# Kernel optimization log

Hardware: AMD Instinct MI355X
Metric: run time of the kernel (lower is better)

The kernel has to match this reference:

```python
import jax, jax.numpy as jnp
import numpy as np

N = 100000   # nodes
E = 1600000  # edges
Q = 500000   # query edges
F = 128      # num_features
H = 256      # hidden_dim
D = 128      # embedding_dim


def setup_inputs() -> dict:
    key = jax.random.key(0)
    ks = jax.random.split(key, 16)

    def lin_w(k, fan_in, fan_out):
        return (jax.random.normal(k, (fan_in, fan_out), jnp.float32)
                / np.float32(np.sqrt(fan_in)))

    inp = {}
    inp['x'] = jax.random.normal(ks[0], (N, F), jnp.float32)
    inp['edge_index'] = jax.random.randint(ks[1], (2, E), 0, N)
    inp['query_edges'] = jax.random.randint(ks[2], (2, Q), 0, N)
    inp['int_values'] = jax.random.randint(ks[3], (N,), 0, 1000000)
    inp['partition_ids'] = jax.random.randint(ks[4], (N,), 0, 1000)
    # GCNConv1 / GCNConv2 / encoder fc
    inp['W1'] = lin_w(ks[5], F, H);  inp['b1'] = jnp.zeros((H,), jnp.float32)
    inp['W2'] = lin_w(ks[6], H, H);  inp['b2'] = jnp.zeros((H,), jnp.float32)
    inp['Wfc'] = lin_w(ks[7], H, D); inp['bfc'] = jnp.zeros((D,), jnp.float32)
    # decoder MLP: in = 2*D + 2
    inp['Wd1'] = lin_w(ks[8], 2 * D + 2, H);    inp['bd1'] = jnp.zeros((H,), jnp.float32)
    inp['Wd2'] = lin_w(ks[9], H, H // 2);       inp['bd2'] = jnp.zeros((H // 2,), jnp.float32)
    inp['Wd3'] = lin_w(ks[10], H // 2, 1);      inp['bd3'] = jnp.zeros((1,), jnp.float32)
    return inp


def reference(x, edge_index, query_edges, int_values, partition_ids,
              W1, b1, W2, b2, Wfc, bfc, Wd1, bd1, Wd2, bd2, Wd3, bd3):
    n = x.shape[0]
    # GCN: add self-loops, symmetric degree normalization
    loop = jnp.arange(n)
    src = jnp.concatenate([edge_index[0], loop])  # [E+N]
    dst = jnp.concatenate([edge_index[1], loop])
    deg = jax.ops.segment_sum(jnp.ones_like(dst, jnp.float32), dst, num_segments=n)
    dinv = jnp.where(deg > 0, jax.lax.rsqrt(deg), 0.0)
    norm = dinv[src] * dinv[dst]  # [E+N]

    def gcn_conv(h, W, b):
        hw = h @ W                                   # [N,out]
        msg = hw[src] * norm[:, None]                # [E+N,out]
        return jax.ops.segment_sum(msg, dst, num_segments=n) + b

    h = jax.nn.relu(gcn_conv(x, W1, b1))
    h = jax.nn.relu(gcn_conv(h, W2, b2))
    z = h @ Wfc + bfc                                # [N,D]

    qs, qd = query_edges[0], query_edges[1]
    z_src = z[qs]                                    # [Q,D]
    z_dst = z[qd]
    int_diff = (int_values[qd] - int_values[qs]).astype(jnp.float32)[:, None]
    same_part = (partition_ids[qs] == partition_ids[qd]).astype(jnp.float32)[:, None]
    zc = jnp.concatenate([z_src, z_dst, int_diff, same_part], axis=-1)  # [Q,2D+2]

    u = jax.nn.relu(zc @ Wd1 + bd1)
    u = jax.nn.relu(u @ Wd2 + bd2)
    out = jax.nn.sigmoid(u @ Wd3 + bd3)
    return out.squeeze(-1)  # [Q]
```

## Files before the change

### kernel.cpp

```cpp
#include <hip/hip_runtime.h>
#include <math.h>


typedef __attribute__((ext_vector_type(8))) short short8;
typedef __attribute__((ext_vector_type(4))) float f32x4;

__device__ __forceinline__ float4 ld4(const float* p){ return *reinterpret_cast<const float4*>(p); }
__device__ __forceinline__ void st4(float* p, float4 v){ *reinterpret_cast<float4*>(p) = v; }
__device__ __forceinline__ unsigned short f2bf(float f){
    union{float f; unsigned u;} v; v.f = f;
    unsigned r = (v.u + 0x7FFFu + ((v.u >> 16) & 1u)) >> 16;
    return (unsigned short)r;
}
__device__ __forceinline__ float bf2f(unsigned short b){
    union{unsigned u; float f;} v; v.u = ((unsigned)b) << 16; return v.f;
}

__global__ void k_count(const int* __restrict__ ei, int E, int* __restrict__ counts){
    int e = blockIdx.x * 256 + threadIdx.x;
    if (e < E) atomicAdd(&counts[ei[E + e]], 1);
}

__global__ __launch_bounds__(1024) void k_blocksum(const int* __restrict__ counts, int n,
                                                   int* __restrict__ bsum){
    __shared__ int sb[1024];
    int i = blockIdx.x * 1024 + threadIdx.x;
    sb[threadIdx.x] = (i < n) ? counts[i] : 0;
    __syncthreads();
    for (int off = 512; off > 0; off >>= 1){
        if (threadIdx.x < off) sb[threadIdx.x] += sb[threadIdx.x + off];
        __syncthreads();
    }
    if (threadIdx.x == 0) bsum[blockIdx.x] = sb[0];
}

__global__ void k_bscan(const int* __restrict__ bsum, int nb,
                        int* __restrict__ boff, int* __restrict__ offsets, int n){
    if (threadIdx.x == 0){
        int run = 0;
        for (int b = 0; b < nb; ++b){ boff[b] = run; run += bsum[b]; }
        offsets[n] = run;
    }
}

__global__ __launch_bounds__(1024) void k_offsets(const int* __restrict__ counts, int n,
                                                  const int* __restrict__ boff,
                                                  int* __restrict__ offsets,
                                                  int* __restrict__ cursor,
                                                  float* __restrict__ dinv){
    __shared__ int sb[1024];
    int i = blockIdx.x * 1024 + threadIdx.x;
    int v = (i < n) ? counts[i] : 0;
    if (i < n) dinv[i] = rsqrtf((float)(v + 1));
    sb[threadIdx.x] = v;
    __syncthreads();
    for (int off = 1; off < 1024; off <<= 1){
        int t = (threadIdx.x >= off) ? sb[threadIdx.x - off] : 0;
        __syncthreads();
        sb[threadIdx.x] += t;
        __syncthreads();
    }
    if (i < n){
        int ex = boff[blockIdx.x] + sb[threadIdx.x] - v;
        offsets[i] = ex; cursor[i] = ex;
    }
}

__global__ void k_fill(const int* __restrict__ ei, int E,
                       int* __restrict__ cursor, int* __restrict__ srclist){
    int e = blockIdx.x * 256 + threadIdx.x;
    if (e < E){
        int s = ei[e], d = ei[E + e];
        int pos = atomicAdd(&cursor[d], 1);
        srclist[pos] = s;
    }
}

__global__ void k_split_w(const float* __restrict__ W, unsigned short* __restrict__ hi,
                          unsigned short* __restrict__ lo, int K, int Nn){
    int id = blockIdx.x * 256 + threadIdx.x;
    if (id >= K * Nn) return;
    int n = id / K, k = id - n * K;
    float v = W[(size_t)k * Nn + n];
    unsigned short h = f2bf(v);
    hi[id] = h;
    lo[id] = f2bf(v - bf2f(h));
}

__global__ void k_split_pack(const float* __restrict__ W, unsigned short* __restrict__ hi,
                             unsigned short* __restrict__ lo, int K, int Nn){
    int idx = blockIdx.x * 256 + threadIdx.x;
    if (idx >= K * Nn) return;
    int j = idx & 7;
    int lane = (idx >> 3) & 63;
    int frag = idx >> 9;
    int kgroups = K >> 5;
    int kg = frag % kgroups;
    int cg = frag / kgroups;
    int c = cg * 16 + (lane & 15);
    int k = kg * 32 + (lane >> 4) * 8 + j;
    float v = W[(size_t)k * Nn + c];
    unsigned short h = f2bf(v);
    hi[idx] = h;
    lo[idx] = f2bf(v - bf2f(h));
}

__global__ void k_scalerows(const float* __restrict__ x, const float* __restrict__ dinv,
                            float* __restrict__ xs, int total4){
    int id = blockIdx.x * 256 + threadIdx.x;
    if (id >= total4) return;
    int node = id >> 5;
    float d = dinv[node];
    float4 v = ld4(&x[(size_t)id * 4]);
    st4(&xs[(size_t)id * 4], make_float4(v.x*d, v.y*d, v.z*d, v.w*d));
}

__global__ __launch_bounds__(256) void k_agg2(const float* __restrict__ in,
        const int* __restrict__ offsets, const int* __restrict__ srclist,
        const float* __restrict__ dinv, float* __restrict__ out, int n){
    int wid = (blockIdx.x * 256 + threadIdx.x) >> 6;
    int lane = threadIdx.x & 63;
    if (wid >= n) return;
    int f = lane * 2;
    float2 acc = *reinterpret_cast<const float2*>(&in[(size_t)wid * 128 + f]);
    int o0 = offsets[wid], o1 = offsets[wid + 1];
    int e = o0;
    for (; e + 3 < o1; e += 4){
        int s0 = srclist[e], s1 = srclist[e+1], s2 = srclist[e+2], s3 = srclist[e+3];
        float2 v0 = *reinterpret_cast<const float2*>(&in[(size_t)s0 * 128 + f]);
        float2 v1 = *reinterpret_cast<const float2*>(&in[(size_t)s1 * 128 + f]);
        float2 v2 = *reinterpret_cast<const float2*>(&in[(size_t)s2 * 128 + f]);
        float2 v3 = *reinterpret_cast<const float2*>(&in[(size_t)s3 * 128 + f]);
        acc.x += (v0.x + v1.x) + (v2.x + v3.x);
        acc.y += (v0.y + v1.y) + (v2.y + v3.y);
    }
    for (; e < o1; ++e){
        int s0 = srclist[e];
        float2 v0 = *reinterpret_cast<const float2*>(&in[(size_t)s0 * 128 + f]);
        acc.x += v0.x; acc.y += v0.y;
    }
    float d = dinv[wid];
    *reinterpret_cast<float2*>(&out[(size_t)wid * 128 + f]) = make_float2(acc.x * d, acc.y * d);
}

__global__ __launch_bounds__(256) void k_agg4(const float* __restrict__ in,
        const int* __restrict__ offsets, const int* __restrict__ srclist,
        const float* __restrict__ dinv, float* __restrict__ out, int n){
    int wid = (blockIdx.x * 256 + threadIdx.x) >> 6;
    int lane = threadIdx.x & 63;
    if (wid >= n) return;
    int f = lane * 4;
    float4 acc = ld4(&in[(size_t)wid * 256 + f]);
    int o0 = offsets[wid], o1 = offsets[wid + 1];
    int e = o0;
    for (; e + 3 < o1; e += 4){
        int s0 = srclist[e], s1 = srclist[e+1], s2 = srclist[e+2], s3 = srclist[e+3];
        float4 v0 = ld4(&in[(size_t)s0 * 256 + f]);
        float4 v1 = ld4(&in[(size_t)s1 * 256 + f]);
        float4 v2 = ld4(&in[(size_t)s2 * 256 + f]);
        float4 v3 = ld4(&in[(size_t)s3 * 256 + f]);
        acc.x += (v0.x + v1.x) + (v2.x + v3.x);
        acc.y += (v0.y + v1.y) + (v2.y + v3.y);
        acc.z += (v0.z + v1.z) + (v2.z + v3.z);
        acc.w += (v0.w + v1.w) + (v2.w + v3.w);
    }
    for (; e < o1; ++e){
        int s0 = srclist[e];
        float4 v0 = ld4(&in[(size_t)s0 * 256 + f]);
        acc.x += v0.x; acc.y += v0.y; acc.z += v0.z; acc.w += v0.w;
    }
    float d = dinv[wid];
    st4(&out[(size_t)wid * 256 + f],
        make_float4(acc.x * d, acc.y * d, acc.z * d, acc.w * d));
}

template<bool RELU, bool POSTSCALE>
__global__ __launch_bounds__(256) void k_mgemm(
        const float* __restrict__ A, const unsigned short* __restrict__ Bh,
        const unsigned short* __restrict__ Bl, const float* __restrict__ bias,
        const float* __restrict__ pscale, float* __restrict__ C,
        int M, int K, int Nn){
    __shared__ unsigned short As_h[128][40], As_l[128][40];
    __shared__ unsigned short Bs_h[128][40], Bs_l[128][40];
    int tid = threadIdx.x;
    int l = tid & 63, w = tid >> 6;
    int wr = w >> 1, wc = w & 1;
    int row0 = blockIdx.x * 128, col0 = blockIdx.y * 128;
    int lr = l & 15, lg = l >> 4, lk = lg * 8;

    f32x4 acc[4][4] = {};

    for (int kt = 0; kt < K; kt += 32){
#pragma unroll
        for (int lp = 0; lp < 4; ++lp){
            int idx = tid + lp * 256;
            int r = idx >> 3, c4 = idx & 7;
            float4 v = make_float4(0.f, 0.f, 0.f, 0.f);
            if (row0 + r < M) v = ld4(&A[(size_t)(row0 + r) * K + kt + c4 * 4]);
            unsigned short h0 = f2bf(v.x), h1 = f2bf(v.y), h2 = f2bf(v.z), h3 = f2bf(v.w);
            unsigned short e0 = f2bf(v.x - bf2f(h0)), e1 = f2bf(v.y - bf2f(h1));
            unsigned short e2 = f2bf(v.z - bf2f(h2)), e3 = f2bf(v.w - bf2f(h3));
            *reinterpret_cast<uint2*>(&As_h[r][c4 * 4]) =
                make_uint2((unsigned)h0 | ((unsigned)h1 << 16), (unsigned)h2 | ((unsigned)h3 << 16));
            *reinterpret_cast<uint2*>(&As_l[r][c4 * 4]) =
                make_uint2((unsigned)e0 | ((unsigned)e1 << 16), (unsigned)e2 | ((unsigned)e3 << 16));
        }
#pragma unroll
        for (int lp = 0; lp < 2; ++lp){
            int idx = tid + lp * 256;
            int r = idx >> 2, c8 = idx & 3;
            size_t go = (size_t)(col0 + r) * K + kt + c8 * 8;
            *reinterpret_cast<uint4*>(&Bs_h[r][c8 * 8]) = *reinterpret_cast<const uint4*>(&Bh[go]);
            *reinterpret_cast<uint4*>(&Bs_l[r][c8 * 8]) = *reinterpret_cast<const uint4*>(&Bl[go]);
        }
        __syncthreads();

        short8 ah[4], al[4], bh[4], bl[4];
#pragma unroll
        for (int mi = 0; mi < 4; ++mi){
            ah[mi] = *reinterpret_cast<const short8*>(&As_h[wr * 64 + mi * 16 + lr][lk]);
            al[mi] = *reinterpret_cast<const short8*>(&As_l[wr * 64 + mi * 16 + lr][lk]);
        }
#pragma unroll
        for (int ni = 0; ni < 4; ++ni){
            bh[ni] = *reinterpret_cast<const short8*>(&Bs_h[wc * 64 + ni * 16 + lr][lk]);
            bl[ni] = *reinterpret_cast<const short8*>(&Bs_l[wc * 64 + ni * 16 + lr][lk]);
        }
#pragma unroll
        for (int mi = 0; mi < 4; ++mi)
#pragma unroll
            for (int ni = 0; ni < 4; ++ni)
                acc[mi][ni] = __builtin_amdgcn_mfma_f32_16x16x32_bf16(ah[mi], bh[ni], acc[mi][ni], 0, 0, 0);
#pragma unroll
        for (int mi = 0; mi < 4; ++mi)
#pragma unroll
            for (int ni = 0; ni < 4; ++ni)
                acc[mi][ni] = __builtin_amdgcn_mfma_f32_16x16x32_bf16(ah[mi], bl[ni], acc[mi][ni], 0, 0, 0);
#pragma unroll
        for (int mi = 0; mi < 4; ++mi)
#pragma unroll
            for (int ni = 0; ni < 4; ++ni)
                acc[mi][ni] = __builtin_amdgcn_mfma_f32_16x16x32_bf16(al[mi], bh[ni], acc[mi][ni], 0, 0, 0);
        __syncthreads();
    }

#pragma unroll
    for (int ni = 0; ni < 4; ++ni){
        int col = col0 + wc * 64 + ni * 16 + lr;
        float bv = bias[col];
#pragma unroll
        for (int mi = 0; mi < 4; ++mi){
#pragma unroll
            for (int rr = 0; rr < 4; ++rr){
                int grow = row0 + wr * 64 + mi * 16 + lg * 4 + rr;
                if (grow < M){
                    float v = acc[mi][ni][rr] + bv;
                    if (RELU) v = fmaxf(v, 0.f);
                    if (POSTSCALE) v *= pscale[grow];
                    C[(size_t)grow * Nn + col] = v;
                }
            }
        }
    }
}

__global__ __launch_bounds__(512, 4) void k_dec(
        const float* __restrict__ z, const int* __restrict__ qe,
        const int* __restrict__ iv, const int* __restrict__ pid,
        const unsigned short* __restrict__ W1h, const unsigned short* __restrict__ W1l,
        const float* __restrict__ Wd1, const float* __restrict__ bd1,
        const unsigned short* __restrict__ W2h, const unsigned short* __restrict__ W2l,
        const float* __restrict__ bd2, const float* __restrict__ Wd3,
        const float* __restrict__ bd3, float* __restrict__ out, int Q){
    __shared__ unsigned short As_h[64][264];
    __shared__ unsigned short As_l[64][264];
    __shared__ int   sQs[64], sQd[64];
    __shared__ float sIdf[64], sSp[64];

    int tid = threadIdx.x;
    int q0 = blockIdx.x * 64;
    if (tid < 64){
        int q = q0 + tid;
        int qs = 0, qd = 0; float idf = 0.f, sp = 0.f;
        if (q < Q){
            qs = qe[q]; qd = qe[Q + q];
            idf = (float)(iv[qd] - iv[qs]);
            sp = (pid[qs] == pid[qd]) ? 1.f : 0.f;
        }
        sQs[tid] = qs; sQd[tid] = qd; sIdf[tid] = idf; sSp[tid] = sp;
    }
    __syncthreads();

#pragma unroll
    for (int lp = 0; lp < 4; ++lp){
        int ch = tid + lp * 512;
        int r = ch >> 5, c8 = ch & 31;
        int srow = (c8 < 16) ? sQs[r] : sQd[r];
        int colb = (c8 & 15) * 8;
        float4 v0 = ld4(&z[(size_t)srow * 128 + colb]);
        float4 v1 = ld4(&z[(size_t)srow * 128 + colb + 4]);
        float vv[8] = {v0.x, v0.y, v0.z, v0.w, v1.x, v1.y, v1.z, v1.w};
        unsigned short hh[8], ll[8];
#pragma unroll
        for (int j = 0; j < 8; ++j){
            hh[j] = f2bf(vv[j]);
            ll[j] = f2bf(vv[j] - bf2f(hh[j]));
        }
        *reinterpret_cast<uint4*>(&As_h[r][c8 * 8]) = *reinterpret_cast<uint4*>(hh);
        *reinterpret_cast<uint4*>(&As_l[r][c8 * 8]) = *reinterpret_cast<uint4*>(ll);
    }
    __syncthreads();

    int l = tid & 63, w = tid >> 6;
    int wr = w >> 2, wc = w & 3;
    int lr = l & 15, lg = l >> 4, lk = lg * 8;

    f32x4 acc1[2][4] = {};
#pragma unroll
    for (int ks = 0; ks < 8; ++ks){
        int kt = ks * 32;
        short8 ah[2], al[2], bh[4], bl[4];
#pragma unroll
        for (int mi = 0; mi < 2; ++mi){
            int row = wr * 32 + mi * 16 + lr;
            ah[mi] = *reinterpret_cast<const short8*>(&As_h[row][kt + lk]);
            al[mi] = *reinterpret_cast<const short8*>(&As_l[row][kt + lk]);
        }
#pragma unroll
        for (int ni = 0; ni < 4; ++ni){
            size_t off = ((size_t)((wc * 4 + ni) * 8 + ks) << 9) + l * 8;
            bh[ni] = *reinterpret_cast<const short8*>(&W1h[off]);
            bl[ni] = *reinterpret_cast<const short8*>(&W1l[off]);
        }
#pragma unroll
        for (int mi = 0; mi < 2; ++mi)
#pragma unroll
            for (int ni = 0; ni < 4; ++ni)
                acc1[mi][ni] = __builtin_amdgcn_mfma_f32_16x16x32_bf16(ah[mi], bh[ni], acc1[mi][ni], 0, 0, 0);
#pragma unroll
        for (int mi = 0; mi < 2; ++mi)
#pragma unroll
            for (int ni = 0; ni < 4; ++ni)
                acc1[mi][ni] = __builtin_amdgcn_mfma_f32_16x16x32_bf16(ah[mi], bl[ni], acc1[mi][ni], 0, 0, 0);
#pragma unroll
        for (int mi = 0; mi < 2; ++mi)
#pragma unroll
            for (int ni = 0; ni < 4; ++ni)
                acc1[mi][ni] = __builtin_amdgcn_mfma_f32_16x16x32_bf16(al[mi], bh[ni], acc1[mi][ni], 0, 0, 0);
    }
    __syncthreads();

#pragma unroll
    for (int ni = 0; ni < 4; ++ni){
        int c = wc * 64 + ni * 16 + lr;
        float bv  = bd1[c];
        float wiv = Wd1[256 * 256 + c];
        float wsv = Wd1[257 * 256 + c];
#pragma unroll
        for (int mi = 0; mi < 2; ++mi){
#pragma unroll
            for (int rr = 0; rr < 4; ++rr){
                int r = wr * 32 + mi * 16 + lg * 4 + rr;
                float u = acc1[mi][ni][rr] + bv + sIdf[r] * wiv + sSp[r] * wsv;
                u = fmaxf(u, 0.f);
                unsigned short h = f2bf(u);
                As_h[r][c] = h;
                As_l[r][c] = f2bf(u - bf2f(h));
            }
        }
    }
    __syncthreads();

    f32x4 acc2[2][2] = {};
#pragma unroll
    for (int ks = 0; ks < 8; ++ks){
        int kt = ks * 32;
        short8 ah[2], al[2], bh[2], bl[2];
#pragma unroll
        for (int mi = 0; mi < 2; ++mi){
            int row = wr * 32 + mi * 16 + lr;
            ah[mi] = *reinterpret_cast<const short8*>(&As_h[row][kt + lk]);
            al[mi] = *reinterpret_cast<const short8*>(&As_l[row][kt + lk]);
        }
#pragma unroll
        for (int ni = 0; ni < 2; ++ni){
            size_t off = ((size_t)((wc * 2 + ni) * 8 + ks) << 9) + l * 8;
            bh[ni] = *reinterpret_cast<const short8*>(&W2h[off]);
            bl[ni] = *reinterpret_cast<const short8*>(&W2l[off]);
        }
#pragma unroll
        for (int mi = 0; mi < 2; ++mi)
#pragma unroll
            for (int ni = 0; ni < 2; ++ni)
                acc2[mi][ni] = __builtin_amdgcn_mfma_f32_16x16x32_bf16(ah[mi], bh[ni], acc2[mi][ni], 0, 0, 0);
#pragma unroll
        for (int mi = 0; mi < 2; ++mi)
#pragma unroll
            for (int ni = 0; ni < 2; ++ni)
                acc2[mi][ni] = __builtin_amdgcn_mfma_f32_16x16x32_bf16(ah[mi], bl[ni], acc2[mi][ni], 0, 0, 0);
#pragma unroll
        for (int mi = 0; mi < 2; ++mi)
#pragma unroll
            for (int ni = 0; ni < 2; ++ni)
                acc2[mi][ni] = __builtin_amdgcn_mfma_f32_16x16x32_bf16(al[mi], bh[ni], acc2[mi][ni], 0, 0, 0);
    }
    __syncthreads();

    float* red = (float*)&As_h[0][0];
    float psum[2][4] = {};
#pragma unroll
    for (int ni = 0; ni < 2; ++ni){
        int c = wc * 32 + ni * 16 + lr;
        float b2v = bd2[c];
        float w3v = Wd3[c];
#pragma unroll
        for (int mi = 0; mi < 2; ++mi)
#pragma unroll
            for (int rr = 0; rr < 4; ++rr)
                psum[mi][rr] += fmaxf(acc2[mi][ni][rr] + b2v, 0.f) * w3v;
    }
#pragma unroll
    for (int mi = 0; mi < 2; ++mi)
#pragma unroll
        for (int rr = 0; rr < 4; ++rr){
            int r = wr * 32 + mi * 16 + lg * 4 + rr;
            red[r * 65 + wc * 16 + lr] = psum[mi][rr];
        }
    __syncthreads();

    {
        int qr = tid >> 3, part = tid & 7;
        float s = 0.f;
#pragma unroll
        for (int j = 0; j < 8; ++j) s += red[qr * 65 + part * 8 + j];
        s += __shfl_xor(s, 1, 8);
        s += __shfl_xor(s, 2, 8);
        s += __shfl_xor(s, 4, 8);
        int q = q0 + qr;
        if (part == 0 && q < Q) out[q] = 1.f / (1.f + expf(-(s + bd3[0])));
    }
}

extern "C" void kernel_launch(void* const* d_in, const int* in_sizes, int n_in,
                              void* d_out, int out_size, void* d_ws, size_t ws_size,
                              hipStream_t stream){
    const float* x   = (const float*)d_in[0];
    const int*   ei  = (const int*)  d_in[1];
    const int*   qe  = (const int*)  d_in[2];
    const int*   iv  = (const int*)  d_in[3];
    const int*   pid = (const int*)  d_in[4];
    const float* W1  = (const float*)d_in[5];
    const float* b1  = (const float*)d_in[6];
    const float* W2  = (const float*)d_in[7];
    const float* b2  = (const float*)d_in[8];
    const float* Wfc = (const float*)d_in[9];
    const float* bfc = (const float*)d_in[10];
    const float* Wd1 = (const float*)d_in[11];
    const float* bd1 = (const float*)d_in[12];
    const float* Wd2 = (const float*)d_in[13];
    const float* bd2 = (const float*)d_in[14];
    const float* Wd3 = (const float*)d_in[15];
    const float* bd3 = (const float*)d_in[16];
    float* out = (float*)d_out;

    const int N = in_sizes[3];
    const int E = in_sizes[1] / 2;
    const int Q = in_sizes[2] / 2;

    char* p = (char*)d_ws;
    auto alloc = [&](size_t bytes) -> char* {
        char* r = p; p += (bytes + 255) & ~(size_t)255; return r;
    };
    int*   counts  = (int*)  alloc((size_t)N * 4);
    int*   offsets = (int*)  alloc((size_t)(N + 1) * 4);
    int*   cursor  = (int*)  alloc((size_t)(N + 1) * 4);
    int*   srclist = (int*)  alloc((size_t)E * 4);
    float* dinv    = (float*)alloc((size_t)N * 4);
    int*   bsum    = (int*)  alloc(1024 * 4);
    int*   boff    = (int*)  alloc(1024 * 4);
    unsigned short* w1h  = (unsigned short*)alloc(256 * 128 * 2);
    unsigned short* w1l  = (unsigned short*)alloc(256 * 128 * 2);
    unsigned short* w2h  = (unsigned short*)alloc(256 * 256 * 2);
    unsigned short* w2l  = (unsigned short*)alloc(256 * 256 * 2);
    unsigned short* wfh  = (unsigned short*)alloc(128 * 256 * 2);
    unsigned short* wfl  = (unsigned short*)alloc(128 * 256 * 2);
    unsigned short* wd1h = (unsigned short*)alloc(256 * 256 * 2);
    unsigned short* wd1l = (unsigned short*)alloc(256 * 256 * 2);
    unsigned short* wd2h = (unsigned short*)alloc(128 * 256 * 2);
    unsigned short* wd2l = (unsigned short*)alloc(128 * 256 * 2);
    float* P1 = (float*)alloc((size_t)N * 256 * 4);
    float* P2 = (float*)alloc((size_t)N * 256 * 4);

    float* xs  = P2;
    float* ag1 = P2 + (size_t)N * 128;
    float* h1s = P1;
    float* ag2 = P2;
    float* h2  = P1;
    float* z   = P2;

    const int nb = (N + 1023) / 1024;
    dim3 blk(256);

    hipMemsetAsync(counts, 0, (size_t)N * 4, stream);
    k_count   <<<dim3((E + 255) / 256), blk,        0, stream>>>(ei, E, counts);
    k_blocksum<<<dim3(nb),              dim3(1024), 0, stream>>>(counts, N, bsum);
    k_bscan   <<<dim3(1),               dim3(64),   0, stream>>>(bsum, nb, boff, offsets, N);
    k_offsets <<<dim3(nb),              dim3(1024), 0, stream>>>(counts, N, boff, offsets, cursor, dinv);
    k_fill    <<<dim3((E + 255) / 256), blk,        0, stream>>>(ei, E, cursor, srclist);

    k_split_w   <<<dim3(128), blk, 0, stream>>>(W1,  w1h,  w1l,  128, 256);
    k_split_w   <<<dim3(256), blk, 0, stream>>>(W2,  w2h,  w2l,  256, 256);
    k_split_w   <<<dim3(128), blk, 0, stream>>>(Wfc, wfh,  wfl,  256, 128);
    k_split_pack<<<dim3(256), blk, 0, stream>>>(Wd1, wd1h, wd1l, 256, 256);
    k_split_pack<<<dim3(128), blk, 0, stream>>>(Wd2, wd2h, wd2l, 256, 128);

    k_scalerows<<<dim3((N * 32 + 255) / 256), blk, 0, stream>>>(x, dinv, xs, N * 32);
    k_agg2<<<dim3(N / 4), blk, 0, stream>>>(xs, offsets, srclist, dinv, ag1, N);
    k_mgemm<true,  true ><<<dim3((N + 127) / 128, 2), blk, 0, stream>>>(ag1, w1h, w1l, b1, dinv, h1s, N, 128, 256);
    k_agg4<<<dim3(N / 4), blk, 0, stream>>>(h1s, offsets, srclist, dinv, ag2, N);
    k_mgemm<true,  false><<<dim3((N + 127) / 128, 2), blk, 0, stream>>>(ag2, w2h, w2l, b2, nullptr, h2, N, 256, 256);
    k_mgemm<false, false><<<dim3((N + 127) / 128, 1), blk, 0, stream>>>(h2, wfh, wfl, bfc, nullptr, z, N, 256, 128);

    k_dec<<<dim3((Q + 63) / 64), dim3(512), 0, stream>>>(z, qe, iv, pid,
                                                         wd1h, wd1l, Wd1, bd1,
                                                         wd2h, wd2l, bd2, Wd3, bd3, out, Q);
}
```

Baseline: 1.220 ms.

## Emit split-bf16 hi/lo activations from producers and fold row scaling into aggregation

Aggregation and GEMM kernels now write activations already split into bf16 hi/lo halves, so the consuming GEMMs and decoder load packed bf16 directly instead of reconverting fp32 every tile. The separate row-scaling kernel is removed and the source-degree scaling moves into the first aggregation's gather loop. This cuts redundant conversion work and one full pass over x. In exchange, the first aggregation does an extra dinv gather per edge, and the intermediate buffer layout is rearranged.

```diff
diff --git a/kernel.cpp b/kernel.cpp
--- a/kernel.cpp
+++ b/kernel.cpp
@@ -105,47 +105,47 @@
     lo[idx] = f2bf(v - bf2f(h));
 }
 
-__global__ void k_scalerows(const float* __restrict__ x, const float* __restrict__ dinv,
-                            float* __restrict__ xs, int total4){
-    int id = blockIdx.x * 256 + threadIdx.x;
-    if (id >= total4) return;
-    int node = id >> 5;
-    float d = dinv[node];
-    float4 v = ld4(&x[(size_t)id * 4]);
-    st4(&xs[(size_t)id * 4], make_float4(v.x*d, v.y*d, v.z*d, v.w*d));
-}
-
-__global__ __launch_bounds__(256) void k_agg2(const float* __restrict__ in,
+__global__ __launch_bounds__(256) void k_agg2(const float* __restrict__ x,
         const int* __restrict__ offsets, const int* __restrict__ srclist,
-        const float* __restrict__ dinv, float* __restrict__ out, int n){
+        const float* __restrict__ dinv,
+        unsigned short* __restrict__ outh, unsigned short* __restrict__ outl, int n){
     int wid = (blockIdx.x * 256 + threadIdx.x) >> 6;
     int lane = threadIdx.x & 63;
     if (wid >= n) return;
     int f = lane * 2;
-    float2 acc = *reinterpret_cast<const float2*>(&in[(size_t)wid * 128 + f]);
+    float dself = dinv[wid];
+    float2 xv = *reinterpret_cast<const float2*>(&x[(size_t)wid * 128 + f]);
+    float2 acc = make_float2(xv.x * dself, xv.y * dself);
     int o0 = offsets[wid], o1 = offsets[wid + 1];
     int e = o0;
     for (; e + 3 < o1; e += 4){
         int s0 = srclist[e], s1 = srclist[e+1], s2 = srclist[e+2], s3 = srclist[e+3];
-        float2 v0 = *reinterpret_cast<const float2*>(&in[(size_t)s0 * 128 + f]);
-        float2 v1 = *reinterpret_cast<const float2*>(&in[(size_t)s1 * 128 + f]);
-        float2 v2 = *reinterpret_cast<const float2*>(&in[(size_t)s2 * 128 + f]);
-        float2 v3 = *reinterpret_cast<const float2*>(&in[(size_t)s3 * 128 + f]);
-        acc.x += (v0.x + v1.x) + (v2.x + v3.x);
-        acc.y += (v0.y + v1.y) + (v2.y + v3.y);
+        float d0 = dinv[s0], d1 = dinv[s1], d2 = dinv[s2], d3 = dinv[s3];
+        float2 v0 = *reinterpret_cast<const float2*>(&x[(size_t)s0 * 128 + f]);
+        float2 v1 = *reinterpret_cast<const float2*>(&x[(size_t)s1 * 128 + f]);
+        float2 v2 = *reinterpret_cast<const float2*>(&x[(size_t)s2 * 128 + f]);
+        float2 v3 = *reinterpret_cast<const float2*>(&x[(size_t)s3 * 128 + f]);
+        acc.x += v0.x * d0 + v1.x * d1 + v2.x * d2 + v3.x * d3;
+        acc.y += v0.y * d0 + v1.y * d1 + v2.y * d2 + v3.y * d3;
     }
     for (; e < o1; ++e){
         int s0 = srclist[e];
-        float2 v0 = *reinterpret_cast<const float2*>(&in[(size_t)s0 * 128 + f]);
-        acc.x += v0.x; acc.y += v0.y;
-    }
-    float d = dinv[wid];
-    *reinterpret_cast<float2*>(&out[(size_t)wid * 128 + f]) = make_float2(acc.x * d, acc.y * d);
+        float d0 = dinv[s0];
+        float2 v0 = *reinterpret_cast<const float2*>(&x[(size_t)s0 * 128 + f]);
+        acc.x += v0.x * d0; acc.y += v0.y * d0;
+    }
+    float vx = acc.x * dself, vy = acc.y * dself;
+    unsigned short hx = f2bf(vx), hy = f2bf(vy);
+    size_t o = (size_t)wid * 128 + f;
+    *reinterpret_cast<unsigned*>(&outh[o]) = (unsigned)hx | ((unsigned)hy << 16);
+    *reinterpret_cast<unsigned*>(&outl[o]) =
+        (unsigned)f2bf(vx - bf2f(hx)) | ((unsigned)f2bf(vy - bf2f(hy)) << 16);
 }
 
 __global__ __launch_bounds__(256) void k_agg4(const float* __restrict__ in,
         const int* __restrict__ offsets, const int* __restrict__ srclist,
-        const float* __restrict__ dinv, float* __restrict__ out, int n){
+        const float* __restrict__ dinv,
+        unsigned short* __restrict__ outh, unsigned short* __restrict__ outl, int n){
     int wid = (blockIdx.x * 256 + threadIdx.x) >> 6;
     int lane = threadIdx.x & 63;
     if (wid >= n) return;
@@ -170,16 +170,27 @@
         acc.x += v0.x; acc.y += v0.y; acc.z += v0.z; acc.w += v0.w;
     }
     float d = dinv[wid];
-    st4(&out[(size_t)wid * 256 + f],
-        make_float4(acc.x * d, acc.y * d, acc.z * d, acc.w * d));
-}
-
-template<bool RELU, bool POSTSCALE>
+    float vv[4] = {acc.x * d, acc.y * d, acc.z * d, acc.w * d};
+    unsigned short hh[4], ll[4];
+#pragma unroll
+    for (int j = 0; j < 4; ++j){
+        hh[j] = f2bf(vv[j]);
+        ll[j] = f2bf(vv[j] - bf2f(hh[j]));
+    }
+    size_t o = (size_t)wid * 256 + f;
+    *reinterpret_cast<uint2*>(&outh[o]) =
+        make_uint2((unsigned)hh[0] | ((unsigned)hh[1] << 16), (unsigned)hh[2] | ((unsigned)hh[3] << 16));
+    *reinterpret_cast<uint2*>(&outl[o]) =
+        make_uint2((unsigned)ll[0] | ((unsigned)ll[1] << 16), (unsigned)ll[2] | ((unsigned)ll[3] << 16));
+}
+
+template<bool RELU, bool POSTSCALE, bool SPLITOUT>
 __global__ __launch_bounds__(256) void k_mgemm(
-        const float* __restrict__ A, const unsigned short* __restrict__ Bh,
-        const unsigned short* __restrict__ Bl, const float* __restrict__ bias,
-        const float* __restrict__ pscale, float* __restrict__ C,
-        int M, int K, int Nn){
+        const unsigned short* __restrict__ Ah, const unsigned short* __restrict__ Al,
+        const unsigned short* __restrict__ Bh, const unsigned short* __restrict__ Bl,
+        const float* __restrict__ bias, const float* __restrict__ pscale,
+        float* __restrict__ C, unsigned short* __restrict__ Ch,
+        unsigned short* __restrict__ Cl, int M, int K, int Nn){
     __shared__ unsigned short As_h[128][40], As_l[128][40];
     __shared__ unsigned short Bs_h[128][40], Bs_l[128][40];
     int tid = threadIdx.x;
@@ -192,18 +203,17 @@
 
     for (int kt = 0; kt < K; kt += 32){
 #pragma unroll
-        for (int lp = 0; lp < 4; ++lp){
+        for (int lp = 0; lp < 2; ++lp){
             int idx = tid + lp * 256;
-            int r = idx >> 3, c4 = idx & 7;
-            float4 v = make_float4(0.f, 0.f, 0.f, 0.f);
-            if (row0 + r < M) v = ld4(&A[(size_t)(row0 + r) * K + kt + c4 * 4]);
-            unsigned short h0 = f2bf(v.x), h1 = f2bf(v.y), h2 = f2bf(v.z), h3 = f2bf(v.w);
-            unsigned short e0 = f2bf(v.x - bf2f(h0)), e1 = f2bf(v.y - bf2f(h1));
-            unsigned short e2 = f2bf(v.z - bf2f(h2)), e3 = f2bf(v.w - bf2f(h3));
-            *reinterpret_cast<uint2*>(&As_h[r][c4 * 4]) =
-                make_uint2((unsigned)h0 | ((unsigned)h1 << 16), (unsigned)h2 | ((unsigned)h3 << 16));
-            *reinterpret_cast<uint2*>(&As_l[r][c4 * 4]) =
-                make_uint2((unsigned)e0 | ((unsigned)e1 << 16), (unsigned)e2 | ((unsigned)e3 << 16));
+            int r = idx >> 2, c8 = idx & 3;
+            size_t go = (size_t)(row0 + r) * K + kt + c8 * 8;
+            uint4 vh = make_uint4(0,0,0,0), vl = make_uint4(0,0,0,0);
+            if (row0 + r < M){
+                vh = *reinterpret_cast<const uint4*>(&Ah[go]);
+                vl = *reinterpret_cast<const uint4*>(&Al[go]);
+            }
+            *reinterpret_cast<uint4*>(&As_h[r][c8 * 8]) = vh;
+            *reinterpret_cast<uint4*>(&As_l[r][c8 * 8]) = vl;
         }
 #pragma unroll
         for (int lp = 0; lp < 2; ++lp){
@@ -257,7 +267,13 @@
                     float v = acc[mi][ni][rr] + bv;
                     if (RELU) v = fmaxf(v, 0.f);
                     if (POSTSCALE) v *= pscale[grow];
-                    C[(size_t)grow * Nn + col] = v;
+                    if (SPLITOUT){
+                        unsigned short h = f2bf(v);
+                        Ch[(size_t)grow * Nn + col] = h;
+                        Cl[(size_t)grow * Nn + col] = f2bf(v - bf2f(h));
+                    } else {
+                        C[(size_t)grow * Nn + col] = v;
+                    }
                 }
             }
         }
@@ -265,7 +281,8 @@
 }
 
 __global__ __launch_bounds__(512, 4) void k_dec(
-        const float* __restrict__ z, const int* __restrict__ qe,
+        const unsigned short* __restrict__ zh, const unsigned short* __restrict__ zl,
+        const int* __restrict__ qe,
         const int* __restrict__ iv, const int* __restrict__ pid,
         const unsigned short* __restrict__ W1h, const unsigned short* __restrict__ W1l,
         const float* __restrict__ Wd1, const float* __restrict__ bd1,
@@ -296,18 +313,9 @@
         int ch = tid + lp * 512;
         int r = ch >> 5, c8 = ch & 31;
         int srow = (c8 < 16) ? sQs[r] : sQd[r];
-        int colb = (c8 & 15) * 8;
-        float4 v0 = ld4(&z[(size_t)srow * 128 + colb]);
-        float4 v1 = ld4(&z[(size_t)srow * 128 + colb + 4]);
-        float vv[8] = {v0.x, v0.y, v0.z, v0.w, v1.x, v1.y, v1.z, v1.w};
-        unsigned short hh[8], ll[8];
-#pragma unroll
-        for (int j = 0; j < 8; ++j){
-            hh[j] = f2bf(vv[j]);
-            ll[j] = f2bf(vv[j] - bf2f(hh[j]));
-        }
-        *reinterpret_cast<uint4*>(&As_h[r][c8 * 8]) = *reinterpret_cast<uint4*>(hh);
-        *reinterpret_cast<uint4*>(&As_l[r][c8 * 8]) = *reinterpret_cast<uint4*>(ll);
+        size_t go = (size_t)srow * 128 + (c8 & 15) * 8;
+        *reinterpret_cast<uint4*>(&As_h[r][c8 * 8]) = *reinterpret_cast<const uint4*>(&zh[go]);
+        *reinterpret_cast<uint4*>(&As_l[r][c8 * 8]) = *reinterpret_cast<const uint4*>(&zl[go]);
     }
     __syncthreads();
 
@@ -488,15 +496,18 @@
     unsigned short* wd1l = (unsigned short*)alloc(256 * 256 * 2);
     unsigned short* wd2h = (unsigned short*)alloc(128 * 256 * 2);
     unsigned short* wd2l = (unsigned short*)alloc(128 * 256 * 2);
-    float* P1 = (float*)alloc((size_t)N * 256 * 4);
-    float* P2 = (float*)alloc((size_t)N * 256 * 4);
-
-    float* xs  = P2;
-    float* ag1 = P2 + (size_t)N * 128;
-    float* h1s = P1;
-    float* ag2 = P2;
-    float* h2  = P1;
-    float* z   = P2;
+    float* PA = (float*)alloc((size_t)N * 256 * 4);
+    unsigned short* PB = (unsigned short*)alloc((size_t)N * 256 * 2 * 2);
+
+    unsigned short* ag1h = PB;
+    unsigned short* ag1l = PB + (size_t)N * 128;
+    float*          h1s  = PA;
+    unsigned short* ag2h = PB;
+    unsigned short* ag2l = PB + (size_t)N * 256;
+    unsigned short* h2h  = (unsigned short*)PA;
+    unsigned short* h2l  = (unsigned short*)PA + (size_t)N * 256;
+    unsigned short* zh   = PB;
+    unsigned short* zl   = PB + (size_t)N * 128;
 
     const int nb = (N + 1023) / 1024;
     dim3 blk(256);
@@ -514,14 +525,16 @@
     k_split_pack<<<dim3(256), blk, 0, stream>>>(Wd1, wd1h, wd1l, 256, 256);
     k_split_pack<<<dim3(128), blk, 0, stream>>>(Wd2, wd2h, wd2l, 256, 128);
 
-    k_scalerows<<<dim3((N * 32 + 255) / 256), blk, 0, stream>>>(x, dinv, xs, N * 32);
-    k_agg2<<<dim3(N / 4), blk, 0, stream>>>(xs, offsets, srclist, dinv, ag1, N);
-    k_mgemm<true,  true ><<<dim3((N + 127) / 128, 2), blk, 0, stream>>>(ag1, w1h, w1l, b1, dinv, h1s, N, 128, 256);
-    k_agg4<<<dim3(N / 4), blk, 0, stream>>>(h1s, offsets, srclist, dinv, ag2, N);
-    k_mgemm<true,  false><<<dim3((N + 127) / 128, 2), blk, 0, stream>>>(ag2, w2h, w2l, b2, nullptr, h2, N, 256, 256);
-    k_mgemm<false, false><<<dim3((N + 127) / 128, 1), blk, 0, stream>>>(h2, wfh, wfl, bfc, nullptr, z, N, 256, 128);
-
-    k_dec<<<dim3((Q + 63) / 64), dim3(512), 0, stream>>>(z, qe, iv, pid,
+    k_agg2<<<dim3(N / 4), blk, 0, stream>>>(x, offsets, srclist, dinv, ag1h, ag1l, N);
+    k_mgemm<true,  true,  false><<<dim3((N + 127) / 128, 2), blk, 0, stream>>>(
+        ag1h, ag1l, w1h, w1l, b1, dinv, h1s, nullptr, nullptr, N, 128, 256);
+    k_agg4<<<dim3(N / 4), blk, 0, stream>>>(h1s, offsets, srclist, dinv, ag2h, ag2l, N);
+    k_mgemm<true,  false, true ><<<dim3((N + 127) / 128, 2), blk, 0, stream>>>(
+        ag2h, ag2l, w2h, w2l, b2, nullptr, nullptr, h2h, h2l, N, 256, 256);
+    k_mgemm<false, false, true ><<<dim3((N + 127) / 128, 1), blk, 0, stream>>>(
+        h2h, h2l, wfh, wfl, bfc, nullptr, nullptr, zh, zl, N, 256, 128);
+
+    k_dec<<<dim3((Q + 63) / 64), dim3(512), 0, stream>>>(zh, zl, qe, iv, pid,
                                                          wd1h, wd1l, Wd1, bd1,
                                                          wd2h, wd2l, bd2, Wd3, bd3, out, Q);
 }
```

New measurement: 1.216 ms. Within noise of the previous version (-0.3%).
